# Kernel optimization log

Hardware: AMD Instinct MI355X
Metric: run time of the kernel (lower is better)

The kernel has to match this reference:

```python
import jax, jax.numpy as jnp
import numpy as np

# XORChainModel.forward: state[0] = inputs[0]; state[i] = state[i-1] ^ inputs[i]
# i.e. a cumulative XOR (inclusive prefix scan with XOR) along the chain axis.
# XOR is associative, so we use jax.lax.associative_scan (log-depth parallel scan).

SEQ_LEN = 4096  # number of steps in the XOR chain (len(inputs) list in torch)
BITS = 8192     # self.bits: width of each bit vector


def setup_inputs() -> dict:
    key = jax.random.key(0)
    # inputs[i] is a 1-D bit vector of length BITS; stack the whole list into [S, BITS]
    inputs = jax.random.randint(key, (SEQ_LEN, BITS), 0, 2, dtype=jnp.int32)
    return {"inputs": inputs}


def reference(inputs):
    # outputs[i] = inputs[0] ^ inputs[1] ^ ... ^ inputs[i]
    # Equivalent to the torch module's list of per-step states, stacked on axis 0.
    return jax.lax.associative_scan(jnp.bitwise_xor, inputs, axis=0)
```

## Files before the change

### kernel.cpp

```cpp
#include <hip/hip_runtime.h>
#include <stdint.h>


#define S 4096
#define B4 2048
#define TPB 512
#define NCT (B4 / TPB)
#define OUTER 64
#define NOUT (S / OUTER)
#define NBLK (NOUT * NCT)
#define NWORDS (NOUT * B4)
#define POISON 0xAAAAAAAAu
#define STG 4
#define NSTG (OUTER / STG)

typedef unsigned int v4u __attribute__((ext_vector_type(4)));
typedef unsigned long long u64;
typedef const __attribute__((address_space(1))) v4u* gp1_t;
typedef __attribute__((address_space(3))) v4u* lp3_t;

__device__ __forceinline__ bool valid(unsigned w) {
    return (w & 0x300u) == 0x100u;
}
__device__ __forceinline__ u64 repl(unsigned nib) {
    u64 m = nib;
    m |= m << 4; m |= m << 8; m |= m << 16; m |= m << 32;
    return m;
}

__global__ __launch_bounds__(TPB) void xor_sc0(
        const v4u* __restrict__ in, v4u* __restrict__ out,
        unsigned* __restrict__ ctl) {
    unsigned* agg = ctl + 64;
    unsigned* inc = agg + NWORDS;

    __shared__ v4u sh[2][STG][TPB];

    const int tid   = (int)threadIdx.x;
    const int bid   = (int)blockIdx.x;
    const int ct    = bid & (NCT - 1);
    const int o     = bid >> 2;
    const int colg  = ct * TPB + tid;
    const int wbase = tid & ~63;

    const v4u* p = in + (size_t)o * OUTER * B4 + colg;

    auto STAGE = [&](int srow, int buf) {
#pragma unroll
        for (int j = 0; j < STG; ++j)
            __builtin_amdgcn_global_load_lds(
                (gp1_t)(const void*)(p + (size_t)(srow + j) * B4),
                (lp3_t)(void*)&sh[buf][j][wbase], 16, 0, 1 );
    };

    u64 q[4] = {0ull, 0ull, 0ull, 0ull};
    STAGE(0, 0);
    STAGE(STG, 1);
#pragma unroll
    for (int s = 0; s < NSTG; ++s) {
        if (s < NSTG - 1) asm volatile("s_waitcnt vmcnt(4)" ::: "memory");
        else              asm volatile("s_waitcnt vmcnt(0)" ::: "memory");
        const int buf = s & 1;
#pragma unroll
        for (int j = 0; j < STG; ++j) {
            v4u v = sh[buf][j][tid];
            unsigned n = (v.x & 1u) | ((v.y & 1u) << 1) |
                         ((v.z & 1u) << 2) | ((v.w & 1u) << 3);
            const int r = s * STG + j;
            q[r >> 4] ^= (u64)n << (4 * (r & 15));
        }
        asm volatile("s_waitcnt lgkmcnt(0)" ::: "memory");
        if (s + 2 < NSTG) STAGE((s + 2) * STG, buf);
    }

    u64 tt = q[0] ^ q[1] ^ q[2] ^ q[3];
    tt ^= tt >> 32; tt ^= tt >> 16; tt ^= tt >> 8; tt ^= tt >> 4;
    const unsigned myagg = (unsigned)tt & 0xFu;
    __hip_atomic_store(&agg[(size_t)o * B4 + colg], 0x100u | myagg,
                       __ATOMIC_RELAXED, __HIP_MEMORY_SCOPE_AGENT);

    unsigned ex = 0u;
    int k = o - 1;
    while (k >= 0) {
        unsigned iw = __hip_atomic_load(&inc[(size_t)k * B4 + colg],
                                        __ATOMIC_RELAXED,
                                        __HIP_MEMORY_SCOPE_AGENT);
        if (valid(iw)) { ex ^= (iw & 0xFu); break; }
        int n = (k + 1 < 16) ? (k + 1) : 16;
        unsigned a[16];
        for (int j = 0; j < n; ++j)
            a[j] = __hip_atomic_load(&agg[(size_t)(k - j) * B4 + colg],
                                     __ATOMIC_RELAXED,
                                     __HIP_MEMORY_SCOPE_AGENT);
        int consumed = 0;
        for (int j = 0; j < n; ++j) {
            if (valid(a[j])) { ex ^= (a[j] & 0xFu); ++consumed; }
            else break;
        }
        k -= consumed;
        if (consumed == 0) __builtin_amdgcn_s_sleep(1);
    }
    __hip_atomic_store(&inc[(size_t)o * B4 + colg], 0x100u | (ex ^ myagg),
                       __ATOMIC_RELAXED, __HIP_MEMORY_SCOPE_AGENT);

    unsigned carry = ex;
    v4u* qo = out + (size_t)o * OUTER * B4 + colg;
#pragma unroll
    for (int kk = 0; kk < 4; ++kk) {
        u64 x = q[kk];
        x ^= x << 4; x ^= x << 8; x ^= x << 16; x ^= x << 32;
        const u64 f = x ^ repl(carry);
        carry ^= (unsigned)(x >> 60) & 0xFu;
#pragma unroll
        for (int j = 0; j < 16; ++j) {
            const unsigned n = (unsigned)(f >> (4 * j)) & 0xFu;
            v4u ov = (v4u){n & 1u, (n >> 1) & 1u, (n >> 2) & 1u, (n >> 3) & 1u};
            __builtin_nontemporal_store(ov, &qo[(size_t)(kk * 16 + j) * B4]);
        }
    }
}

extern "C" void kernel_launch(void* const* d_in, const int* in_sizes, int n_in,
                              void* d_out, int out_size, void* d_ws, size_t ws_size,
                              hipStream_t stream) {
    const v4u* in = (const v4u*)d_in[0];
    v4u* out = (v4u*)d_out;
    unsigned* ctl = (unsigned*)d_ws;

    xor_sc0<<<NBLK, TPB, 0, stream>>>(in, out, ctl);
}
```

Baseline: 237.6 us.

## Give each block a full row chunk and pack four column carries per word

Each block now owns 16 full rows across all 2048 vector columns, instead of 64 rows of one 512-column stripe. Each thread handles four column groups and packs their 4-bit aggregates into one 16-bit lookback word. Loads and stores now cover whole contiguous rows, and the number of lookback descriptors per chunk drops. The cost is a longer chain of 256 serially dependent chunks in the decoupled lookback, where before there were 64 chunks across 4 independent column stripes.

New measurement: 239.0 us. Within noise of the previous version (+0.6%).

```diff
diff --git a/kernel.cpp b/kernel.cpp
--- a/kernel.cpp
+++ b/kernel.cpp
@@ -5,22 +5,18 @@
 #define S 4096
 #define B4 2048
 #define TPB 512
-#define NCT (B4 / TPB)
-#define OUTER 64
-#define NOUT (S / OUTER)
-#define NBLK (NOUT * NCT)
-#define NWORDS (NOUT * B4)
+#define CHROWS 16
+#define NOUT (S / CHROWS)
+#define NBLK NOUT
 #define POISON 0xAAAAAAAAu
-#define STG 4
-#define NSTG (OUTER / STG)
 
 typedef unsigned int v4u __attribute__((ext_vector_type(4)));
 typedef unsigned long long u64;
 typedef const __attribute__((address_space(1))) v4u* gp1_t;
 typedef __attribute__((address_space(3))) v4u* lp3_t;
 
-__device__ __forceinline__ bool valid(unsigned w) {
-    return (w & 0x300u) == 0x100u;
+__device__ __forceinline__ bool validw(unsigned w) {
+    return (w & 0xFFFF0000u) == 0x00010000u;
 }
 __device__ __forceinline__ u64 repl(unsigned nib) {
     u64 m = nib;
@@ -28,94 +24,97 @@
     return m;
 }
 
-__global__ __launch_bounds__(TPB) void xor_sc0(
+__global__ __launch_bounds__(TPB) void xor_contig(
         const v4u* __restrict__ in, v4u* __restrict__ out,
         unsigned* __restrict__ ctl) {
     unsigned* agg = ctl + 64;
-    unsigned* inc = agg + NWORDS;
+    unsigned* inc = agg + (size_t)NOUT * TPB;
 
-    __shared__ v4u sh[2][STG][TPB];
+    __shared__ v4u lds[2][4][TPB];
 
     const int tid   = (int)threadIdx.x;
-    const int bid   = (int)blockIdx.x;
-    const int ct    = bid & (NCT - 1);
-    const int o     = bid >> 2;
-    const int colg  = ct * TPB + tid;
+    const int o     = (int)blockIdx.x;
     const int wbase = tid & ~63;
 
-    const v4u* p = in + (size_t)o * OUTER * B4 + colg;
+    const v4u* base = in + (size_t)o * CHROWS * B4;
 
-    auto STAGE = [&](int srow, int buf) {
+    auto STAGE = [&](int row, int buf) {
 #pragma unroll
-        for (int j = 0; j < STG; ++j)
+        for (int k = 0; k < 4; ++k)
             __builtin_amdgcn_global_load_lds(
-                (gp1_t)(const void*)(p + (size_t)(srow + j) * B4),
-                (lp3_t)(void*)&sh[buf][j][wbase], 16, 0, 1 );
+                (gp1_t)(const void*)(base + (size_t)row * B4 + k * TPB + tid),
+                (lp3_t)(void*)&lds[buf][k][wbase], 16, 0, 0);
     };
 
     u64 q[4] = {0ull, 0ull, 0ull, 0ull};
     STAGE(0, 0);
-    STAGE(STG, 1);
+    STAGE(1, 1);
 #pragma unroll
-    for (int s = 0; s < NSTG; ++s) {
-        if (s < NSTG - 1) asm volatile("s_waitcnt vmcnt(4)" ::: "memory");
-        else              asm volatile("s_waitcnt vmcnt(0)" ::: "memory");
+    for (int s = 0; s < CHROWS; ++s) {
+        if (s < CHROWS - 1) asm volatile("s_waitcnt vmcnt(4)" ::: "memory");
+        else                asm volatile("s_waitcnt vmcnt(0)" ::: "memory");
         const int buf = s & 1;
 #pragma unroll
-        for (int j = 0; j < STG; ++j) {
-            v4u v = sh[buf][j][tid];
+        for (int k = 0; k < 4; ++k) {
+            v4u v = lds[buf][k][tid];
             unsigned n = (v.x & 1u) | ((v.y & 1u) << 1) |
                          ((v.z & 1u) << 2) | ((v.w & 1u) << 3);
-            const int r = s * STG + j;
-            q[r >> 4] ^= (u64)n << (4 * (r & 15));
+            q[k] ^= (u64)n << (4 * s);
         }
         asm volatile("s_waitcnt lgkmcnt(0)" ::: "memory");
-        if (s + 2 < NSTG) STAGE((s + 2) * STG, buf);
+        if (s + 2 < CHROWS) STAGE(s + 2, buf);
     }
 
-    u64 tt = q[0] ^ q[1] ^ q[2] ^ q[3];
-    tt ^= tt >> 32; tt ^= tt >> 16; tt ^= tt >> 8; tt ^= tt >> 4;
-    const unsigned myagg = (unsigned)tt & 0xFu;
-    __hip_atomic_store(&agg[(size_t)o * B4 + colg], 0x100u | myagg,
+    unsigned agg16 = 0u;
+#pragma unroll
+    for (int k = 0; k < 4; ++k) {
+        u64 tt = q[k];
+        tt ^= tt >> 32; tt ^= tt >> 16; tt ^= tt >> 8; tt ^= tt >> 4;
+        agg16 |= ((unsigned)tt & 0xFu) << (4 * k);
+    }
+    __hip_atomic_store(&agg[(size_t)o * TPB + tid], 0x00010000u | agg16,
                        __ATOMIC_RELAXED, __HIP_MEMORY_SCOPE_AGENT);
 
-    unsigned ex = 0u;
+    unsigned ex16 = 0u;
     int k = o - 1;
     while (k >= 0) {
-        unsigned iw = __hip_atomic_load(&inc[(size_t)k * B4 + colg],
+        unsigned iw = __hip_atomic_load(&inc[(size_t)k * TPB + tid],
                                         __ATOMIC_RELAXED,
                                         __HIP_MEMORY_SCOPE_AGENT);
-        if (valid(iw)) { ex ^= (iw & 0xFu); break; }
+        if (validw(iw)) { ex16 ^= (iw & 0xFFFFu); break; }
         int n = (k + 1 < 16) ? (k + 1) : 16;
         unsigned a[16];
         for (int j = 0; j < n; ++j)
-            a[j] = __hip_atomic_load(&agg[(size_t)(k - j) * B4 + colg],
+            a[j] = __hip_atomic_load(&agg[(size_t)(k - j) * TPB + tid],
                                      __ATOMIC_RELAXED,
                                      __HIP_MEMORY_SCOPE_AGENT);
         int consumed = 0;
         for (int j = 0; j < n; ++j) {
-            if (valid(a[j])) { ex ^= (a[j] & 0xFu); ++consumed; }
+            if (validw(a[j])) { ex16 ^= (a[j] & 0xFFFFu); ++consumed; }
             else break;
         }
         k -= consumed;
         if (consumed == 0) __builtin_amdgcn_s_sleep(1);
     }
-    __hip_atomic_store(&inc[(size_t)o * B4 + colg], 0x100u | (ex ^ myagg),
+    __hip_atomic_store(&inc[(size_t)o * TPB + tid],
+                       0x00010000u | (ex16 ^ agg16),
                        __ATOMIC_RELAXED, __HIP_MEMORY_SCOPE_AGENT);
 
-    unsigned carry = ex;
-    v4u* qo = out + (size_t)o * OUTER * B4 + colg;
+    u64 f[4];
 #pragma unroll
     for (int kk = 0; kk < 4; ++kk) {
         u64 x = q[kk];
         x ^= x << 4; x ^= x << 8; x ^= x << 16; x ^= x << 32;
-        const u64 f = x ^ repl(carry);
-        carry ^= (unsigned)(x >> 60) & 0xFu;
+        f[kk] = x ^ repl((ex16 >> (4 * kk)) & 0xFu);
+    }
+    v4u* ob = out + (size_t)o * CHROWS * B4;
 #pragma unroll
-        for (int j = 0; j < 16; ++j) {
-            const unsigned n = (unsigned)(f >> (4 * j)) & 0xFu;
+    for (int j = 0; j < CHROWS; ++j) {
+#pragma unroll
+        for (int kk = 0; kk < 4; ++kk) {
+            const unsigned n = (unsigned)(f[kk] >> (4 * j)) & 0xFu;
             v4u ov = (v4u){n & 1u, (n >> 1) & 1u, (n >> 2) & 1u, (n >> 3) & 1u};
-            __builtin_nontemporal_store(ov, &qo[(size_t)(kk * 16 + j) * B4]);
+            __builtin_nontemporal_store(ov, &ob[(size_t)j * B4 + kk * TPB + tid]);
         }
     }
 }
@@ -127,5 +126,5 @@
     v4u* out = (v4u*)d_out;
     unsigned* ctl = (unsigned*)d_ws;
 
-    xor_sc0<<<NBLK, TPB, 0, stream>>>(in, out, ctl);
+    xor_contig<<<NBLK, TPB, 0, stream>>>(in, out, ctl);
 }
```
